# Kernel tuning notes

Measured on AMD Instinct MI355X. Metric: run time of the kernel, lower is better.

Reference implementation:

```python
import jax, jax.numpy as jnp
import numpy as np

ALPHA = 50.0
EPS = 1e-12  # torch F.normalize eps


def setup_inputs() -> dict:
    key = jax.random.key(0)
    k1, k2 = jax.random.split(key)
    N, C, H, W_sp, K = 64, 128, 64, 64, 64
    x = jax.random.normal(k1, (N, C, H, W_sp), dtype=jnp.float32)
    # centroids.permute(1,0): shape [C, K]; orthogonal-ish init approximated by scaled gaussian
    W = jax.random.normal(k2, (C, K), dtype=jnp.float32) * (1.0 / np.sqrt(C))
    bias = jnp.zeros((K,), dtype=jnp.float32)
    return {"x": x, "W": W, "bias": bias}


def _l2norm(v, axis):
    return v / jnp.maximum(jnp.linalg.norm(v, axis=axis, keepdims=True), EPS)


def reference(x, W, bias):
    N, C, H, W_sp = x.shape
    K = W.shape[1]
    x = _l2norm(x, axis=1)                      # normalize over channels
    xf = x.reshape(N, C, H * W_sp)              # [N, C, P]
    Wn = _l2norm(W, axis=0)                     # column-normalized weight [C, K]
    # soft assignment logits, computed directly in [N, K, P] layout
    sa_logits = jnp.einsum('ncp,ck->nkp', xf, Wn)
    sa = jax.nn.softmax((sa_logits + bias[None, :, None]) * ALPHA, axis=1)  # over clusters
    # VLAD via two GEMM-like contractions instead of the [N,K,C,P] residual tensor:
    # vlad[n,k,c] = sum_p sa[n,k,p] * xf[n,c,p] - W[c,k] * sum_p sa[n,k,p]
    vlad = jnp.einsum('nkp,ncp->nkc', sa, xf) - sa.sum(axis=-1)[:, :, None] * W.T[None]
    vlad = _l2norm(vlad, axis=2)                # intra-normalize per cluster
    vlad = vlad.reshape(N, K * C)
    vlad = _l2norm(vlad, axis=1)                # global L2
    return (vlad, sa_logits)                    # original returns soft_assign_ permuted to [N, K, P]
```

## Files before the change

kernel.cpp:

```cpp
#include <hip/hip_runtime.h>
#include <math.h>

#define ALPHA 50.0f
#define EPS 1e-12f

constexpr int N = 64, C = 128, P = 4096, K = 64;
constexpr int NCH2 = 8;

typedef short short8_t __attribute__((ext_vector_type(8)));
typedef short short4_t __attribute__((ext_vector_type(4)));
typedef float f4 __attribute__((ext_vector_type(4)));

__device__ __forceinline__ unsigned short f2bf(float f) {
    union { float f; unsigned u; } v; v.f = f;
    unsigned r = (v.u + 0x7FFFu + ((v.u >> 16) & 1u)) >> 16;
    return (unsigned short)r;
}

__global__ __launch_bounds__(256) void k_prep(
    const float* __restrict__ W, unsigned short* __restrict__ wnT)
{
    __shared__ float Wl[C * 65];
    __shared__ float cinv[K];
    const int tid = threadIdx.x;
    for (int idx = tid; idx < C * K; idx += 256) {
        int c = idx >> 6, k = idx & 63;
        Wl[c * 65 + k] = W[idx];
    }
    __syncthreads();
    if (tid < K) {
        float s = 0.f;
        for (int c = 0; c < C; ++c) { float v = Wl[c * 65 + tid]; s = fmaf(v, v, s); }
        cinv[tid] = 1.0f / fmaxf(sqrtf(s), EPS);
    }
    __syncthreads();
    for (int idx = tid; idx < K * C; idx += 256) {
        int k = idx >> 7, c = idx & 127;
        wnT[idx] = f2bf(Wl[c * 65 + k] * cinv[k]);
    }
}

__global__ __launch_bounds__(256) void k_fused(
    const float* __restrict__ x, const unsigned short* __restrict__ wnT,
    const float* __restrict__ bias, float* __restrict__ logits,
    float* __restrict__ vlad_part, float* __restrict__ Spart)
{
    __shared__ unsigned short xsT[64 * 136];
    __shared__ unsigned short xsN[128 * 76];
    __shared__ float          saf[64 * 66];
    __shared__ unsigned short sa2s[64 * 72];
    __shared__ float invs[64];
    __shared__ float rfin[64];
    __shared__ float red[256];
    __shared__ float biass[64];

    const int tid  = threadIdx.x;
    const int n    = blockIdx.x >> 3;
    const int blk8 = blockIdx.x & 7;
    const int pbase = blk8 * 512;

    const int w = tid >> 6, lane = tid & 63;
    const int q = lane >> 4, l15 = lane & 15;
    const int pxg = tid & 15, cg = tid >> 4;
    const int px = tid & 63, sq = tid >> 6;

    if (tid < K) biass[tid] = bias[tid];

    short8_t af[4];
    #pragma unroll
    for (int c0 = 0; c0 < 4; ++c0)
        af[c0] = *(const short8_t*)&wnT[(16 * w + l15) * 128 + c0 * 32 + 8 * q];

    f4 acc2[8];
    #pragma unroll
    for (int ct = 0; ct < 8; ++ct) acc2[ct] = (f4){0.f, 0.f, 0.f, 0.f};
    float Sreg = 0.f;

    for (int ch = 0; ch < 8; ++ch) {
        const int p0 = pbase + ch * 64;
        __syncthreads();

        const float* xb = x + (size_t)n * C * P + p0 + 4 * pxg;
        float4 v[8];
        #pragma unroll
        for (int j = 0; j < 8; ++j) v[j] = *(const float4*)&xb[(size_t)(8 * cg + j) * P];
        const float* vf = (const float*)v;

        float pss[4] = {0.f, 0.f, 0.f, 0.f};
        #pragma unroll
        for (int j = 0; j < 8; ++j)
            #pragma unroll
            for (int i = 0; i < 4; ++i)
                pss[i] = fmaf(vf[j * 4 + i], vf[j * 4 + i], pss[i]);
        float* red2 = saf;
        #pragma unroll
        for (int i = 0; i < 4; ++i) red2[(4 * pxg + i) * 16 + cg] = pss[i];

        #pragma unroll
        for (int i = 0; i < 4; ++i) {
            short8_t t;
            #pragma unroll
            for (int j = 0; j < 8; ++j) t[j] = (short)f2bf(vf[j * 4 + i]);
            *(short8_t*)&xsT[(4 * pxg + i) * 136 + 8 * cg] = t;
        }
        #pragma unroll
        for (int j = 0; j < 8; ++j) {
            short4_t t4;
            #pragma unroll
            for (int i = 0; i < 4; ++i) t4[i] = (short)f2bf(vf[j * 4 + i]);
            *(short4_t*)&xsN[(8 * cg + j) * 76 + 4 * pxg] = t4;
        }
        __syncthreads();
        if (tid < 64) {
            float s = 0.f;
            #pragma unroll
            for (int g = 0; g < 16; ++g) s += red2[tid * 16 + g];
            invs[tid] = 1.0f / fmaxf(sqrtf(s), EPS);
        }
        __syncthreads();

        f4 acc1[4];
        #pragma unroll
        for (int t = 0; t < 4; ++t) acc1[t] = (f4){0.f, 0.f, 0.f, 0.f};
        #pragma unroll
        for (int c0 = 0; c0 < 4; ++c0)
            #pragma unroll
            for (int pxt = 0; pxt < 4; ++pxt) {
                short8_t bf = *(const short8_t*)&xsT[(pxt * 16 + l15) * 136 + c0 * 32 + 8 * q];
                acc1[pxt] = __builtin_amdgcn_mfma_f32_16x16x32_bf16(af[c0], bf, acc1[pxt], 0, 0, 0);
            }

        float* lgp = logits + (size_t)n * K * P + p0;
        #pragma unroll
        for (int pxt = 0; pxt < 4; ++pxt) {
            const int pxl = pxt * 16 + l15;
            const float iv = invs[pxl];
            #pragma unroll
            for (int r = 0; r < 4; ++r) {
                const int k = 16 * w + 4 * q + r;
                const float lv = acc1[pxt][r] * iv;
                saf[k * 66 + pxl] = lv;
                lgp[(size_t)k * P + pxl] = lv;
            }
        }
        __syncthreads();

        float ps = 0.f;
        #pragma unroll
        for (int kk = 0; kk < 16; ++kk) {
            const int k = sq * 16 + kk;
            float e = __expf((saf[k * 66 + px] + biass[k]) * ALPHA);
            saf[k * 66 + px] = e;
            ps += e;
        }
        red[tid] = ps;
        __syncthreads();
        if (tid < 64)
            rfin[tid] = 1.0f / (red[tid] + red[64 + tid] + red[128 + tid] + red[192 + tid]);
        __syncthreads();

        {
            float s = 0.f;
            #pragma unroll
            for (int ii = 0; ii < 16; ++ii)
                s += saf[px * 66 + sq * 16 + ii] * rfin[sq * 16 + ii];
            Sreg += s;
        }
        {
            const float rf = rfin[px] * invs[px];
            #pragma unroll
            for (int kk = 0; kk < 16; ++kk) {
                const int k = sq * 16 + kk;
                sa2s[k * 72 + px] = f2bf(saf[k * 66 + px] * rf);
            }
        }
        __syncthreads();

        short8_t a2[2];
        #pragma unroll
        for (int kit = 0; kit < 2; ++kit)
            a2[kit] = *(const short8_t*)&sa2s[(16 * w + l15) * 72 + kit * 32 + 8 * q];
        #pragma unroll
        for (int ct = 0; ct < 8; ++ct)
            #pragma unroll
            for (int kit = 0; kit < 2; ++kit) {
                const unsigned short* bp = &xsN[(ct * 16 + l15) * 76 + kit * 32 + 8 * q];
                short4_t b0 = *(const short4_t*)bp;
                short4_t b1 = *(const short4_t*)(bp + 4);
                short8_t bb;
                bb[0] = b0[0]; bb[1] = b0[1]; bb[2] = b0[2]; bb[3] = b0[3];
                bb[4] = b1[0]; bb[5] = b1[1]; bb[6] = b1[2]; bb[7] = b1[3];
                acc2[ct] = __builtin_amdgcn_mfma_f32_16x16x32_bf16(a2[kit], bb, acc2[ct], 0, 0, 0);
            }
    }

    float* vp = vlad_part + ((size_t)blk8 * N + n) * (size_t)(K * C);
    #pragma unroll
    for (int ct = 0; ct < 8; ++ct)
        #pragma unroll
        for (int r = 0; r < 4; ++r)
            vp[(16 * w + 4 * q + r) * C + ct * 16 + l15] = acc2[ct][r];

    red[tid] = Sreg;
    __syncthreads();
    if (tid < 64)
        Spart[((size_t)blk8 * N + n) * K + tid] =
            red[tid] + red[64 + tid] + red[128 + tid] + red[192 + tid];
}

__global__ __launch_bounds__(256) void k_post(
    const float* __restrict__ vlad_part, const float* __restrict__ W,
    const float* __restrict__ Spart, float* __restrict__ out)
{
    __shared__ float red[256];
    const int tid = threadIdx.x;
    const int n = blockIdx.x;
    const int k = tid >> 2;
    const int part = tid & 3;
    const int c0 = part * 32;

    float Sk = 0.f;
    #pragma unroll
    for (int ch = 0; ch < NCH2; ++ch) Sk += Spart[(size_t)(ch * N + n) * K + k];

    float v[32];
    #pragma unroll
    for (int l = 0; l < 32; ++l) v[l] = 0.f;
    #pragma unroll
    for (int ch = 0; ch < NCH2; ++ch) {
        const float* vp = vlad_part + ((size_t)(ch * N + n) * K + k) * C + c0;
        #pragma unroll
        for (int l4 = 0; l4 < 8; ++l4) {
            float4 t = *(const float4*)&vp[4 * l4];
            v[4 * l4 + 0] += t.x; v[4 * l4 + 1] += t.y;
            v[4 * l4 + 2] += t.z; v[4 * l4 + 3] += t.w;
        }
    }

    float ss = 0.f;
    #pragma unroll
    for (int l = 0; l < 32; ++l) {
        float val = v[l] - W[(size_t)(c0 + l) * K + k] * Sk;
        v[l] = val;
        ss = fmaf(val, val, ss);
    }
    ss += __shfl_xor(ss, 1);
    ss += __shfl_xor(ss, 2);
    const float inv1 = 1.0f / fmaxf(sqrtf(ss), EPS);
    float ss2 = 0.f;
    #pragma unroll
    for (int l = 0; l < 32; ++l) { v[l] *= inv1; ss2 = fmaf(v[l], v[l], ss2); }
    red[tid] = ss2;
    __syncthreads();
    for (int s = 128; s > 0; s >>= 1) {
        if (tid < s) red[tid] += red[tid + s];
        __syncthreads();
    }
    const float inv2 = 1.0f / fmaxf(sqrtf(red[0]), EPS);
    float* op = out + (size_t)n * K * C + k * C + c0;
    #pragma unroll
    for (int l = 0; l < 32; ++l) op[l] = v[l] * inv2;
}

extern "C" void kernel_launch(void* const* d_in, const int* in_sizes, int n_in,
                              void* d_out, int out_size, void* d_ws, size_t ws_size,
                              hipStream_t stream)
{
    const float* x    = (const float*)d_in[0];
    const float* W    = (const float*)d_in[1];
    const float* bias = (const float*)d_in[2];

    float* out_vlad   = (float*)d_out;
    float* out_logits = (float*)d_out + (size_t)N * K * C;

    unsigned short* wnT = (unsigned short*)d_ws;
    float* Spart        = (float*)((char*)d_ws + 32768);
    float* vlad_part    = (float*)((char*)d_ws + 32768 + 131072);

    k_prep<<<dim3(1), dim3(256), 0, stream>>>(W, wnT);
    k_fused<<<dim3(N * NCH2), dim3(256), 0, stream>>>(x, wnT, bias, out_logits, vlad_part, Spart);
    k_post<<<dim3(N), dim3(256), 0, stream>>>(vlad_part, W, Spart, out_vlad);
}
```

Measured before the change: 251.8 us.

## Prefetch next x chunk, fuse exp into logits epilogue, split post into parallel kernels

After: 241.9 us. -3.9%, faster.

```diff
diff --git a/kernel.cpp b/kernel.cpp
--- a/kernel.cpp
+++ b/kernel.cpp
@@ -10,6 +10,8 @@
 typedef short short8_t __attribute__((ext_vector_type(8)));
 typedef short short4_t __attribute__((ext_vector_type(4)));
 typedef float f4 __attribute__((ext_vector_type(4)));
+typedef unsigned int u32x4 __attribute__((ext_vector_type(4)));
+typedef unsigned int u32x2 __attribute__((ext_vector_type(2)));
 
 __device__ __forceinline__ unsigned short f2bf(float f) {
     union { float f; unsigned u; } v; v.f = f;
@@ -17,22 +19,45 @@
     return (unsigned short)r;
 }
 
+__device__ __forceinline__ unsigned cvtpk(float lo, float hi) {
+    unsigned r;
+    asm("v_cvt_pk_bf16_f32 %0, %1, %2" : "=v"(r) : "v"(lo), "v"(hi));
+    return r;
+}
+
+__device__ __forceinline__ void bar_lds() {
+    asm volatile("s_waitcnt lgkmcnt(0)" ::: "memory");
+    __builtin_amdgcn_s_barrier();
+}
+
 __global__ __launch_bounds__(256) void k_prep(
-    const float* __restrict__ W, unsigned short* __restrict__ wnT)
+    const float* __restrict__ W, unsigned short* __restrict__ wnT,
+    float* __restrict__ ss2acc)
 {
     __shared__ float Wl[C * 65];
+    __shared__ float red[256];
     __shared__ float cinv[K];
     const int tid = threadIdx.x;
+    if (tid < K) ss2acc[tid] = 0.f;
     for (int idx = tid; idx < C * K; idx += 256) {
         int c = idx >> 6, k = idx & 63;
         Wl[c * 65 + k] = W[idx];
     }
     __syncthreads();
-    if (tid < K) {
+    {
+        const int k = tid & 63, part = tid >> 6;
         float s = 0.f;
-        for (int c = 0; c < C; ++c) { float v = Wl[c * 65 + tid]; s = fmaf(v, v, s); }
-        cinv[tid] = 1.0f / fmaxf(sqrtf(s), EPS);
-    }
+        #pragma unroll
+        for (int i = 0; i < 32; ++i) {
+            float v = Wl[(part * 32 + i) * 65 + k];
+            s = fmaf(v, v, s);
+        }
+        red[tid] = s;
+    }
+    __syncthreads();
+    if (tid < K)
+        cinv[tid] = 1.0f / fmaxf(
+            sqrtf(red[tid] + red[64 + tid] + red[128 + tid] + red[192 + tid]), EPS);
     __syncthreads();
     for (int idx = tid; idx < K * C; idx += 256) {
         int k = idx >> 7, c = idx & 127;
@@ -40,7 +65,7 @@
     }
 }
 
-__global__ __launch_bounds__(256) void k_fused(
+__global__ __launch_bounds__(256, 2) void k_fused(
     const float* __restrict__ x, const unsigned short* __restrict__ wnT,
     const float* __restrict__ bias, float* __restrict__ logits,
     float* __restrict__ vlad_part, float* __restrict__ Spart)
@@ -49,6 +74,7 @@
     __shared__ unsigned short xsN[128 * 76];
     __shared__ float          saf[64 * 66];
     __shared__ unsigned short sa2s[64 * 72];
+    __shared__ float denom[16][65];
     __shared__ float invs[64];
     __shared__ float rfin[64];
     __shared__ float red[256];
@@ -64,7 +90,7 @@
     const int pxg = tid & 15, cg = tid >> 4;
     const int px = tid & 63, sq = tid >> 6;
 
-    if (tid < K) biass[tid] = bias[tid];
+    if (tid < K) biass[tid] = bias[tid] * ALPHA;
 
     short8_t af[4];
     #pragma unroll
@@ -76,15 +102,22 @@
     for (int ct = 0; ct < 8; ++ct) acc2[ct] = (f4){0.f, 0.f, 0.f, 0.f};
     float Sreg = 0.f;
 
+    const float* xrow = x + (size_t)n * C * P + pbase + 4 * pxg;
+
+    float4 va[8], vb[8];
+    #pragma unroll
+    for (int j = 0; j < 8; ++j) va[j] = *(const float4*)&xrow[(size_t)(8 * cg + j) * P];
+
     for (int ch = 0; ch < 8; ++ch) {
+        if (ch < 7) {
+            const float* xb = xrow + (ch + 1) * 64;
+            #pragma unroll
+            for (int j = 0; j < 8; ++j)
+                vb[j] = *(const float4*)&xb[(size_t)(8 * cg + j) * P];
+        }
+        bar_lds();
         const int p0 = pbase + ch * 64;
-        __syncthreads();
-
-        const float* xb = x + (size_t)n * C * P + p0 + 4 * pxg;
-        float4 v[8];
-        #pragma unroll
-        for (int j = 0; j < 8; ++j) v[j] = *(const float4*)&xb[(size_t)(8 * cg + j) * P];
-        const float* vf = (const float*)v;
+        const float* vf = (const float*)va;
 
         float pss[4] = {0.f, 0.f, 0.f, 0.f};
         #pragma unroll
@@ -98,26 +131,27 @@
 
         #pragma unroll
         for (int i = 0; i < 4; ++i) {
-            short8_t t;
-            #pragma unroll
-            for (int j = 0; j < 8; ++j) t[j] = (short)f2bf(vf[j * 4 + i]);
-            *(short8_t*)&xsT[(4 * pxg + i) * 136 + 8 * cg] = t;
+            u32x4 t;
+            #pragma unroll
+            for (int jj = 0; jj < 4; ++jj)
+                t[jj] = cvtpk(vf[(2 * jj) * 4 + i], vf[(2 * jj + 1) * 4 + i]);
+            *(u32x4*)&xsT[(4 * pxg + i) * 136 + 8 * cg] = t;
         }
         #pragma unroll
         for (int j = 0; j < 8; ++j) {
-            short4_t t4;
-            #pragma unroll
-            for (int i = 0; i < 4; ++i) t4[i] = (short)f2bf(vf[j * 4 + i]);
-            *(short4_t*)&xsN[(8 * cg + j) * 76 + 4 * pxg] = t4;
-        }
-        __syncthreads();
+            u32x2 t;
+            t[0] = cvtpk(vf[j * 4 + 0], vf[j * 4 + 1]);
+            t[1] = cvtpk(vf[j * 4 + 2], vf[j * 4 + 3]);
+            *(u32x2*)&xsN[(8 * cg + j) * 76 + 4 * pxg] = t;
+        }
+        bar_lds();
         if (tid < 64) {
             float s = 0.f;
             #pragma unroll
             for (int g = 0; g < 16; ++g) s += red2[tid * 16 + g];
             invs[tid] = 1.0f / fmaxf(sqrtf(s), EPS);
         }
-        __syncthreads();
+        bar_lds();
 
         f4 acc1[4];
         #pragma unroll
@@ -131,33 +165,33 @@
             }
 
         float* lgp = logits + (size_t)n * K * P + p0;
+        float bz[4];
+        #pragma unroll
+        for (int r = 0; r < 4; ++r) bz[r] = biass[16 * w + 4 * q + r];
         #pragma unroll
         for (int pxt = 0; pxt < 4; ++pxt) {
             const int pxl = pxt * 16 + l15;
             const float iv = invs[pxl];
+            float psum = 0.f;
             #pragma unroll
             for (int r = 0; r < 4; ++r) {
                 const int k = 16 * w + 4 * q + r;
                 const float lv = acc1[pxt][r] * iv;
-                saf[k * 66 + pxl] = lv;
                 lgp[(size_t)k * P + pxl] = lv;
+                const float e = __expf(fmaf(lv, ALPHA, bz[r]));
+                saf[k * 66 + pxl] = e;
+                psum += e;
             }
-        }
-        __syncthreads();
-
-        float ps = 0.f;
-        #pragma unroll
-        for (int kk = 0; kk < 16; ++kk) {
-            const int k = sq * 16 + kk;
-            float e = __expf((saf[k * 66 + px] + biass[k]) * ALPHA);
-            saf[k * 66 + px] = e;
-            ps += e;
-        }
-        red[tid] = ps;
-        __syncthreads();
-        if (tid < 64)
-            rfin[tid] = 1.0f / (red[tid] + red[64 + tid] + red[128 + tid] + red[192 + tid]);
-        __syncthreads();
+            denom[4 * w + q][pxl] = psum;
+        }
+        bar_lds();
+        if (tid < 64) {
+            float d = 0.f;
+            #pragma unroll
+            for (int g = 0; g < 16; ++g) d += denom[g][tid];
+            rfin[tid] = 1.0f / d;
+        }
+        bar_lds();
 
         {
             float s = 0.f;
@@ -174,7 +208,7 @@
                 sa2s[k * 72 + px] = f2bf(saf[k * 66 + px] * rf);
             }
         }
-        __syncthreads();
+        bar_lds();
 
         short8_t a2[2];
         #pragma unroll
@@ -192,6 +226,11 @@
                 bb[4] = b1[0]; bb[5] = b1[1]; bb[6] = b1[2]; bb[7] = b1[3];
                 acc2[ct] = __builtin_amdgcn_mfma_f32_16x16x32_bf16(a2[kit], bb, acc2[ct], 0, 0, 0);
             }
+
+        if (ch < 7) {
+            #pragma unroll
+            for (int j = 0; j < 8; ++j) va[j] = vb[j];
+        }
     }
 
     float* vp = vlad_part + ((size_t)blk8 * N + n) * (size_t)(K * C);
@@ -208,58 +247,82 @@
             red[tid] + red[64 + tid] + red[128 + tid] + red[192 + tid];
 }
 
-__global__ __launch_bounds__(256) void k_post(
+__global__ __launch_bounds__(256) void k_post1(
     const float* __restrict__ vlad_part, const float* __restrict__ W,
-    const float* __restrict__ Spart, float* __restrict__ out)
-{
-    __shared__ float red[256];
+    const float* __restrict__ Spart, float* __restrict__ out,
+    float* __restrict__ ss2acc)
+{
+    __shared__ float red[16];
     const int tid = threadIdx.x;
-    const int n = blockIdx.x;
-    const int k = tid >> 2;
-    const int part = tid & 3;
-    const int c0 = part * 32;
+    const int n  = blockIdx.x >> 2;
+    const int kq = blockIdx.x & 3;
+    const int kl = tid >> 4;
+    const int ci = tid & 15;
+    const int k  = kq * 16 + kl;
+    const int c0 = ci * 8;
 
     float Sk = 0.f;
     #pragma unroll
     for (int ch = 0; ch < NCH2; ++ch) Sk += Spart[(size_t)(ch * N + n) * K + k];
 
-    float v[32];
-    #pragma unroll
-    for (int l = 0; l < 32; ++l) v[l] = 0.f;
+    float v[8];
+    #pragma unroll
+    for (int l = 0; l < 8; ++l) v[l] = 0.f;
     #pragma unroll
     for (int ch = 0; ch < NCH2; ++ch) {
         const float* vp = vlad_part + ((size_t)(ch * N + n) * K + k) * C + c0;
-        #pragma unroll
-        for (int l4 = 0; l4 < 8; ++l4) {
-            float4 t = *(const float4*)&vp[4 * l4];
-            v[4 * l4 + 0] += t.x; v[4 * l4 + 1] += t.y;
-            v[4 * l4 + 2] += t.z; v[4 * l4 + 3] += t.w;
-        }
+        float4 a = *(const float4*)&vp[0];
+        float4 b = *(const float4*)&vp[4];
+        v[0] += a.x; v[1] += a.y; v[2] += a.z; v[3] += a.w;
+        v[4] += b.x; v[5] += b.y; v[6] += b.z; v[7] += b.w;
     }
 
     float ss = 0.f;
     #pragma unroll
-    for (int l = 0; l < 32; ++l) {
+    for (int l = 0; l < 8; ++l) {
         float val = v[l] - W[(size_t)(c0 + l) * K + k] * Sk;
         v[l] = val;
         ss = fmaf(val, val, ss);
     }
     ss += __shfl_xor(ss, 1);
     ss += __shfl_xor(ss, 2);
+    ss += __shfl_xor(ss, 4);
+    ss += __shfl_xor(ss, 8);
     const float inv1 = 1.0f / fmaxf(sqrtf(ss), EPS);
     float ss2 = 0.f;
     #pragma unroll
-    for (int l = 0; l < 32; ++l) { v[l] *= inv1; ss2 = fmaf(v[l], v[l], ss2); }
-    red[tid] = ss2;
-    __syncthreads();
-    for (int s = 128; s > 0; s >>= 1) {
-        if (tid < s) red[tid] += red[tid + s];
-        __syncthreads();
-    }
-    const float inv2 = 1.0f / fmaxf(sqrtf(red[0]), EPS);
-    float* op = out + (size_t)n * K * C + k * C + c0;
-    #pragma unroll
-    for (int l = 0; l < 32; ++l) op[l] = v[l] * inv2;
+    for (int l = 0; l < 8; ++l) { v[l] *= inv1; ss2 = fmaf(v[l], v[l], ss2); }
+    ss2 += __shfl_xor(ss2, 1);
+    ss2 += __shfl_xor(ss2, 2);
+    ss2 += __shfl_xor(ss2, 4);
+    ss2 += __shfl_xor(ss2, 8);
+    if (ci == 0) red[kl] = ss2;
+    __syncthreads();
+    if (tid == 0) {
+        float t = 0.f;
+        #pragma unroll
+        for (int i = 0; i < 16; ++i) t += red[i];
+        atomicAdd(&ss2acc[n], t);
+    }
+
+    float* op = out + (size_t)n * K * C + (size_t)k * C + c0;
+    *(float4*)&op[0] = (float4){v[0], v[1], v[2], v[3]};
+    *(float4*)&op[4] = (float4){v[4], v[5], v[6], v[7]};
+}
+
+__global__ __launch_bounds__(256) void k_post2(
+    float* __restrict__ out, const float* __restrict__ ss2acc)
+{
+    const int n   = blockIdx.x >> 2;
+    const int seg = blockIdx.x & 3;
+    const float inv2 = 1.0f / fmaxf(sqrtf(ss2acc[n]), EPS);
+    float* p = out + (size_t)n * K * C + (size_t)seg * 2048 + (size_t)threadIdx.x * 8;
+    float4 a = *(const float4*)&p[0];
+    float4 b = *(const float4*)&p[4];
+    a.x *= inv2; a.y *= inv2; a.z *= inv2; a.w *= inv2;
+    b.x *= inv2; b.y *= inv2; b.z *= inv2; b.w *= inv2;
+    *(float4*)&p[0] = a;
+    *(float4*)&p[4] = b;
 }
 
 extern "C" void kernel_launch(void* const* d_in, const int* in_sizes, int n_in,
@@ -274,10 +337,12 @@
     float* out_logits = (float*)d_out + (size_t)N * K * C;
 
     unsigned short* wnT = (unsigned short*)d_ws;
+    float* ss2acc       = (float*)((char*)d_ws + 16384);
     float* Spart        = (float*)((char*)d_ws + 32768);
     float* vlad_part    = (float*)((char*)d_ws + 32768 + 131072);
 
-    k_prep<<<dim3(1), dim3(256), 0, stream>>>(W, wnT);
+    k_prep<<<dim3(1), dim3(256), 0, stream>>>(W, wnT, ss2acc);
     k_fused<<<dim3(N * NCH2), dim3(256), 0, stream>>>(x, wnT, bias, out_logits, vlad_part, Spart);
-    k_post<<<dim3(N), dim3(256), 0, stream>>>(vlad_part, W, Spart, out_vlad);
-}
+    k_post1<<<dim3(N * 4), dim3(256), 0, stream>>>(vlad_part, W, Spart, out_vlad, ss2acc);
+    k_post2<<<dim3(N * 4), dim3(256), 0, stream>>>(out_vlad, ss2acc);
+}
```
